# Optimization experiments

Hardware: AMD Instinct MI355X
Metric: run time of the kernel (lower is better)

## Reference

```python
import jax, jax.numpy as jnp
import numpy as np

B, T, C, H = 8, 2048, 384, 64

def setup_inputs() -> dict:
    key = jax.random.key(0)
    k1, k2, k3, k4 = jax.random.split(key, 4)
    x = jax.random.normal(k1, (B, T, C), dtype=jnp.float32)
    Wq = jax.random.normal(k2, (C, H), dtype=jnp.float32) * (C ** -0.5)
    Wk = jax.random.normal(k3, (C, H), dtype=jnp.float32) * (C ** -0.5)
    Wv = jax.random.normal(k4, (C, H), dtype=jnp.float32) * (C ** -0.5)
    return {"x": x, "Wq": Wq, "Wk": Wk, "Wv": Wv}

def reference(x, Wq, Wk, Wv):
    # x: (B, T, C); projections: (B, T, H)
    Bn, Tn, Cn = x.shape
    q = jnp.einsum('btc,ch->bth', x, Wq)
    k = jnp.einsum('btc,ch->bth', x, Wk)
    v = jnp.einsum('btc,ch->bth', x, Wv)
    # NOTE: source scales by C**-0.5 (embedding dim), not head_size**-0.5
    weights = jnp.einsum('bth,bsh->bts', q, k) * (Cn ** -0.5)  # (B, T, T)
    causal = jnp.tril(jnp.ones((Tn, Tn), dtype=bool))
    weights = jnp.where(causal, weights, -jnp.inf)
    # NOTE: source applies softmax over dim=1 (query/row axis), reproduced faithfully
    weights = jax.nn.softmax(weights, axis=1)
    # dropout omitted (eval-mode reference)
    return jnp.einsum('bts,bsh->bth', weights, v)
```

## Files before the change

### kernel.cpp

```cpp
#include <hip/hip_runtime.h>
#include <hip/hip_bf16.h>
#include <math.h>

#define Bn 8
#define Tn 2048
#define Cn 384
#define Hn 64
#define SCALE2 0.07362241f

using bf16x8 = __attribute__((ext_vector_type(8))) short;
using f32x4  = __attribute__((ext_vector_type(4))) float;
using u32x4  = __attribute__((ext_vector_type(4))) unsigned;

#define MFMA(a, b, c) __builtin_amdgcn_mfma_f32_16x16x32_bf16((a), (b), (c), 0, 0, 0)

static __device__ __forceinline__ short f2bf(float f) {
  unsigned u = __float_as_uint(f);
  u += 0x7fffu + ((u >> 16) & 1u);
  return (short)(u >> 16);
}
static __device__ __forceinline__ float bf2f(short s) {
  return __uint_as_float(((unsigned)(unsigned short)s) << 16);
}
static __device__ __forceinline__ float fexp2(float x) {
#if __has_builtin(__builtin_amdgcn_exp2f)
  return __builtin_amdgcn_exp2f(x);
#else
  return exp2f(x);
#endif
}
static __device__ __forceinline__ float frcp(float x) {
#if __has_builtin(__builtin_amdgcn_rcpf)
  return __builtin_amdgcn_rcpf(x);
#else
  return 1.0f / x;
#endif
}
static __device__ __forceinline__ unsigned pack2(float lo, float hi) {
  return (unsigned)(unsigned short)f2bf(lo) | ((unsigned)(unsigned short)f2bf(hi) << 16);
}
static __device__ __forceinline__ bf16x8 ldp(const unsigned* p) {
  u32x4 t; t[0] = p[0]; t[1] = p[1]; t[2] = p[2]; t[3] = p[3];
  return __builtin_bit_cast(bf16x8, t);
}

__global__ __launch_bounds__(256) void wconv_kernel(
    const float* __restrict__ Wq, const float* __restrict__ Wk,
    const float* __restrict__ Wv, short* __restrict__ WbT,
    float* __restrict__ Lsum) {
  int idx = blockIdx.x * 256 + threadIdx.x;
  if (idx < Bn * Tn) Lsum[idx] = 0.f;
  int n = idx / 384, k = idx - n * 384;
  const float* W = (n < 64) ? Wq : (n < 128) ? Wk : Wv;
  WbT[idx] = f2bf(W[k * 64 + (n & 63)]);
}

__global__ __launch_bounds__(256) void proj_kernel(
    const float* __restrict__ x, const short* __restrict__ WbT,
    short* __restrict__ qb, short* __restrict__ kb, short* __restrict__ vT) {
  __shared__ short xs[16][392];
  __shared__ short vtile[64][20];
  const int tid = threadIdx.x;
  const int t0 = blockIdx.x * 16;
  const float* xb = x + (size_t)t0 * Cn;
  #pragma unroll
  for (int i = 0; i < 6; ++i) {
    int j = tid + i * 256;
    int row = j / 96, colv = (j - row * 96) * 4;
    float4 v = *(const float4*)(xb + row * Cn + colv);
    short4 s4; s4.x = f2bf(v.x); s4.y = f2bf(v.y); s4.z = f2bf(v.z); s4.w = f2bf(v.w);
    *(short4*)(&xs[row][colv]) = s4;
  }
  __syncthreads();
  const int w = tid >> 6, l15 = tid & 15, quad = (tid & 63) >> 4;
  f32x4 acc[3] = {};
  for (int ks = 0; ks < 12; ++ks) {
    bf16x8 a = *(const bf16x8*)(&xs[l15][ks * 32 + quad * 8]);
    #pragma unroll
    for (int cf = 0; cf < 3; ++cf) {
      bf16x8 bfr = *(const bf16x8*)(WbT + (size_t)(48 * w + 16 * cf + l15) * Cn + ks * 32 + quad * 8);
      acc[cf] = MFMA(a, bfr, acc[cf]);
    }
  }
  #pragma unroll
  for (int cf = 0; cf < 3; ++cf) {
    int cbase = 48 * w + 16 * cf, c = cbase + l15;
    #pragma unroll
    for (int r = 0; r < 4; ++r) {
      int row = t0 + quad * 4 + r;
      short val = f2bf(acc[cf][r]);
      if (cbase < 64)       qb[(size_t)row * Hn + c] = val;
      else if (cbase < 128) kb[(size_t)row * Hn + (c - 64)] = val;
      else                  vtile[c - 128][quad * 4 + r] = val;
    }
  }
  __syncthreads();
  const int b = t0 >> 11, t0l = t0 & 2047;
  int h = tid >> 2, tseg = (tid & 3) * 4;
  *(short4*)(vT + ((size_t)(b * Hn + h)) * Tn + t0l + tseg) =
      *(const short4*)(&vtile[h][tseg]);
}

__global__ __launch_bounds__(256) void colstats_kernel(
    const short* __restrict__ qb, const short* __restrict__ kb,
    float* __restrict__ Lsum) {
  const int unit = ((blockIdx.x & 7) << 7) | (blockIdx.x >> 3);
  const int b = unit >> 7, rem = unit & 127;
  const int j = rem >> 3, u = rem & 7;
  const int lo = (u * 33) >> 3, hi = ((u + 1) * 33) >> 3;
  const int big = 32 - j;
  const int tid = threadIdx.x, w = tid >> 6, l15 = tid & 15, quad = (tid & 63) >> 4;
  __shared__ float redl[64][17];

  auto run = [&](const int i, const int k0, const int k1) {
    const int s0 = i << 6;
    float l[4] = {0.f, 0.f, 0.f, 0.f};
    const int n = k1 - k0;
    if (n > 0) {
      bf16x8 bk[8];
      #pragma unroll
      for (int nf = 0; nf < 4; ++nf) {
        const size_t krow = (size_t)(b * Tn + s0 + 16 * nf + l15) * Hn;
        bk[2 * nf]     = *(const bf16x8*)(kb + krow + quad * 8);
        bk[2 * nf + 1] = *(const bf16x8*)(kb + krow + 32 + quad * 8);
      }
      auto cload = [&](bf16x8& A0, bf16x8& A1, int k) {
        size_t ar = (size_t)(b * Tn + ((i + k) << 6) + 16 * w + l15) * Hn;
        A0 = *(const bf16x8*)(qb + ar + quad * 8);
        A1 = *(const bf16x8*)(qb + ar + 32 + quad * 8);
      };
      auto ccomp = [&](bf16x8 A0, bf16x8 A1, int k) {
        f32x4 sc[4] = {};
        #pragma unroll
        for (int nf = 0; nf < 4; ++nf) {
          sc[nf] = MFMA(A0, bk[2 * nf], sc[nf]);
          sc[nf] = MFMA(A1, bk[2 * nf + 1], sc[nf]);
        }
        const bool diag = (k == 0);
        const int tb = ((i + k) << 6) + 16 * w + quad * 4;
        #pragma unroll
        for (int nf = 0; nf < 4; ++nf) {
          int s = s0 + 16 * nf + l15;
          #pragma unroll
          for (int r = 0; r < 4; ++r) {
            float v = sc[nf][r] * SCALE2;
            if (diag && (tb + r) < s) v = -INFINITY;
            l[nf] += fexp2(v);
          }
        }
      };
      bf16x8 a0A, a1A, a0B, a1B, a0C, a1C;
      cload(a0A, a1A, k0);
      if (n > 1) cload(a0B, a1B, k0 + 1);
      if (n > 2) cload(a0C, a1C, k0 + 2);
      int k = k0;
      while (k + 3 < k1) {
        ccomp(a0A, a1A, k);     cload(a0A, a1A, k + 3);
        ccomp(a0B, a1B, k + 1); if (k + 4 < k1) cload(a0B, a1B, k + 4);
        ccomp(a0C, a1C, k + 2); if (k + 5 < k1) cload(a0C, a1C, k + 5);
        k += 3;
      }
      const int rem2 = k1 - k;
      if (rem2 > 0) ccomp(a0A, a1A, k);
      if (rem2 > 1) ccomp(a0B, a1B, k + 1);
      if (rem2 > 2) ccomp(a0C, a1C, k + 2);
    }
    __syncthreads();
    #pragma unroll
    for (int nf = 0; nf < 4; ++nf) redl[16 * nf + l15][w * 4 + quad] = l[nf];
    __syncthreads();
    if (tid < 64) {
      float ls = 0.f;
      #pragma unroll
      for (int q2 = 0; q2 < 16; ++q2) ls += redl[tid][q2];
      atomicAdd(&Lsum[b * Tn + s0 + tid], ls);
    }
  };
  run(j, lo, min(hi, big));
  run(31 - j, max(lo, big) - big, hi - big);
}

__global__ __launch_bounds__(256, 2) void outg_kernel(
    const short* __restrict__ qb, const short* __restrict__ kb,
    const short* __restrict__ vT, const float* __restrict__ Lsum,
    float* __restrict__ out) {
  const int bid = blockIdx.x;
  const int b = bid & 7;
  const int rest = bid >> 3;
  const int tile = 31 - (rest >> 1);
  const int half = rest & 1;
  const int nch = tile + 1;
  const int tid = threadIdx.x, w = tid >> 6, l15 = tid & 15, quad = (tid & 63) >> 4;
  __shared__ unsigned plds[4][512];
  __shared__ float red[4][32][64];
  __shared__ float rcpl[2048];

  const int smax = nch << 6;
  for (int s = tid; s < smax; s += 256)
    rcpl[s] = frcp(Lsum[b * Tn + s]);
  __syncthreads();

  const int swz = (l15 & 7) << 4;
  int wroff[8];
  #pragma unroll
  for (int nf = 0; nf < 4; ++nf)
    #pragma unroll
    for (int p = 0; p < 2; ++p)
      wroff[2 * nf + p] = (l15 * 128 + ((nf * 32 + quad * 8 + p * 4) ^ swz)) >> 2;
  const int rd0 = (l15 * 128 + ((quad * 16) ^ swz)) >> 2;
  const int rd1 = (l15 * 128 + ((64 + quad * 16) ^ swz)) >> 2;
  const size_t QKbase = (size_t)b * Tn * Hn;
  const size_t Vbase  = (size_t)b * Hn * Tn;
  const int tbase = (tile << 6) + (half << 5);
  const int tg0 = tbase + l15;
  const int tg1 = tbase + 16 + l15;

  const size_t qrow0 = QKbase + (size_t)(tbase + l15) * Hn;
  const size_t qrow1 = qrow0 + 16 * Hn;
  const bf16x8 qf00 = *(const bf16x8*)(qb + qrow0 + quad * 8);
  const bf16x8 qf01 = *(const bf16x8*)(qb + qrow0 + 32 + quad * 8);
  const bf16x8 qf10 = *(const bf16x8*)(qb + qrow1 + quad * 8);
  const bf16x8 qf11 = *(const bf16x8*)(qb + qrow1 + 32 + quad * 8);

  f32x4 acc0[4] = {}, acc1[4] = {};
  bf16x8 kfA[8], kfB[8], vf[8];
  auto loadK = [&](bf16x8 (&kf)[8], int ch) {
    const int s0 = ch << 6;
    #pragma unroll
    for (int nf = 0; nf < 4; ++nf) {
      const size_t kr = QKbase + (size_t)(s0 + 16 * nf + l15) * Hn;
      kf[2 * nf]     = *(const bf16x8*)(kb + kr + quad * 8);
      kf[2 * nf + 1] = *(const bf16x8*)(kb + kr + 32 + quad * 8);
    }
  };
  auto loadV = [&](int ch) {
    const int s0 = ch << 6;
    #pragma unroll
    for (int nf = 0; nf < 4; ++nf) {
      const size_t vr = Vbase + (size_t)(16 * nf + l15) * Tn + s0;
      vf[2 * nf]     = *(const bf16x8*)(vT + vr + quad * 8);
      vf[2 * nf + 1] = *(const bf16x8*)(vT + vr + 32 + quad * 8);
    }
  };
  auto strip = [&](const f32x4 (&sc)[4], const float (&rl)[16], int s0,
                   bool diag, int tg, f32x4 (&acc)[4]) {
    #pragma unroll
    for (int nf = 0; nf < 4; ++nf) {
      float ev[4];
      #pragma unroll
      for (int r = 0; r < 4; ++r) {
        float v = sc[nf][r] * SCALE2;
        const int s = s0 + 16 * nf + quad * 4 + r;
        if (diag && tg < s) v = -INFINITY;
        ev[r] = fexp2(v) * rl[nf * 4 + r];
      }
      plds[w][wroff[2 * nf]]     = pack2(ev[0], ev[1]);
      plds[w][wroff[2 * nf + 1]] = pack2(ev[2], ev[3]);
    }
    const bf16x8 a0 = ldp(&plds[w][rd0]);
    const bf16x8 a1 = ldp(&plds[w][rd1]);
    __builtin_amdgcn_s_setprio(1);
    #pragma unroll
    for (int nf = 0; nf < 4; ++nf) {
      acc[nf] = MFMA(a0, vf[2 * nf], acc[nf]);
      acc[nf] = MFMA(a1, vf[2 * nf + 1], acc[nf]);
    }
    __builtin_amdgcn_s_setprio(0);
  };
  auto body = [&](int ch, const bf16x8 (&CUR)[8], bf16x8 (&NXT)[8]) {
    const int s0 = ch << 6;
    const int nx = ch + 4;
    f32x4 sc0[4] = {}, sc1[4] = {};
    __builtin_amdgcn_s_setprio(1);
    #pragma unroll
    for (int nf = 0; nf < 4; ++nf) {
      sc0[nf] = MFMA(CUR[2 * nf], qf00, sc0[nf]);
      sc0[nf] = MFMA(CUR[2 * nf + 1], qf01, sc0[nf]);
    }
    #pragma unroll
    for (int nf = 0; nf < 4; ++nf) {
      sc1[nf] = MFMA(CUR[2 * nf], qf10, sc1[nf]);
      sc1[nf] = MFMA(CUR[2 * nf + 1], qf11, sc1[nf]);
    }
    __builtin_amdgcn_s_setprio(0);
    if (nx < nch) loadK(NXT, nx);
    float rl[16];
    #pragma unroll
    for (int nf = 0; nf < 4; ++nf)
      #pragma unroll
      for (int r = 0; r < 4; ++r)
        rl[nf * 4 + r] = rcpl[s0 + 16 * nf + quad * 4 + r];
    const bool diag = (ch == tile);
    strip(sc0, rl, s0, diag, tg0, acc0);
    strip(sc1, rl, s0, diag, tg1, acc1);
    if (nx < nch) loadV(nx);
  };

  if (w < nch) { loadK(kfA, w); loadV(w); }
  for (int ch = w; ch < nch; ch += 8) {
    body(ch, kfA, kfB);
    if (ch + 4 < nch) body(ch + 4, kfB, kfA);
  }

  #pragma unroll
  for (int nf = 0; nf < 4; ++nf)
    #pragma unroll
    for (int r = 0; r < 4; ++r) {
      red[w][quad * 4 + r][16 * nf + l15]      = acc0[nf][r];
      red[w][16 + quad * 4 + r][16 * nf + l15] = acc1[nf][r];
    }
  __syncthreads();
  {
    const int row = tid >> 3, c8 = (tid & 7) * 8;
    float4 t0 = {0.f, 0.f, 0.f, 0.f}, t1 = {0.f, 0.f, 0.f, 0.f};
    #pragma unroll
    for (int ww = 0; ww < 4; ++ww) {
      float4 s0 = *(const float4*)(&red[ww][row][c8]);
      float4 s1 = *(const float4*)(&red[ww][row][c8 + 4]);
      t0.x += s0.x; t0.y += s0.y; t0.z += s0.z; t0.w += s0.w;
      t1.x += s1.x; t1.y += s1.y; t1.z += s1.z; t1.w += s1.w;
    }
    float* o = &out[QKbase + (size_t)(tbase + row) * Hn + c8];
    *(float4*)(o) = t0;
    *(float4*)(o + 4) = t1;
  }
}

extern "C" void kernel_launch(void* const* d_in, const int* in_sizes, int n_in,
                              void* d_out, int out_size, void* d_ws, size_t ws_size,
                              hipStream_t stream) {
  const float* x  = (const float*)d_in[0];
  const float* Wq = (const float*)d_in[1];
  const float* Wk = (const float*)d_in[2];
  const float* Wv = (const float*)d_in[3];
  char* ws = (char*)d_ws;
  short* qb   = (short*)(ws);
  short* kb   = (short*)(ws + 2097152);
  short* vT   = (short*)(ws + 4194304);
  short* WbT  = (short*)(ws + 6291456);
  float* Lsum = (float*)(ws + 6438912);
  float* outp = (float*)d_out;

  hipLaunchKernelGGL(wconv_kernel, dim3(288), dim3(256), 0, stream, Wq, Wk, Wv, WbT, Lsum);
  hipLaunchKernelGGL(proj_kernel, dim3(Bn * Tn / 16), dim3(256), 0, stream, x, WbT, qb, kb, vT);
  hipLaunchKernelGGL(colstats_kernel, dim3(1024), dim3(256), 0, stream, qb, kb, Lsum);
  hipLaunchKernelGGL(outg_kernel, dim3(512), dim3(256), 0, stream, qb, kb, vT, Lsum, outp);
}
```

Measured before the change: 132.0 us.

## Fuse column-stats and output kernels via grid barrier, keeping exp scores in registers

The separate column-sum and output kernels are merged into one persistent attention kernel of 512 blocks with 512 threads. Each block computes QK^T once, keeps the bf16 exponentials in registers, reduces column sums through LDS atomics and then global atomics, waits at a software grid barrier, and does the PV pass using the stored exponentials. This avoids recomputing QK^T and exp in a second kernel and removes one launch. The softmax scale is folded into Wq during weight conversion. The cost is heavy register pressure, a grid-wide spin barrier that needs all 512 blocks resident at once (risk of deadlock or stalls), and extra bf16 rounding of unnormalized exponentials.

```diff
diff --git a/kernel.cpp b/kernel.cpp
--- a/kernel.cpp
+++ b/kernel.cpp
@@ -7,6 +7,7 @@
 #define Cn 384
 #define Hn 64
 #define SCALE2 0.07362241f
+#define NBLK 512
 
 using bf16x8 = __attribute__((ext_vector_type(8))) short;
 using f32x4  = __attribute__((ext_vector_type(4))) float;
@@ -18,9 +19,6 @@
   unsigned u = __float_as_uint(f);
   u += 0x7fffu + ((u >> 16) & 1u);
   return (short)(u >> 16);
-}
-static __device__ __forceinline__ float bf2f(short s) {
-  return __uint_as_float(((unsigned)(unsigned short)s) << 16);
 }
 static __device__ __forceinline__ float fexp2(float x) {
 #if __has_builtin(__builtin_amdgcn_exp2f)
@@ -43,16 +41,30 @@
   u32x4 t; t[0] = p[0]; t[1] = p[1]; t[2] = p[2]; t[3] = p[3];
   return __builtin_bit_cast(bf16x8, t);
 }
+static __device__ __forceinline__ void grid_barrier(unsigned* cnt) {
+  __syncthreads();
+  if (threadIdx.x == 0) {
+    __threadfence();
+    atomicAdd(cnt, 1u);
+    while (__hip_atomic_load(cnt, __ATOMIC_ACQUIRE, __HIP_MEMORY_SCOPE_AGENT)
+           < (unsigned)NBLK)
+      __builtin_amdgcn_s_sleep(8);
+  }
+  __syncthreads();
+}
 
 __global__ __launch_bounds__(256) void wconv_kernel(
     const float* __restrict__ Wq, const float* __restrict__ Wk,
     const float* __restrict__ Wv, short* __restrict__ WbT,
-    float* __restrict__ Lsum) {
+    float* __restrict__ Lsum, unsigned* __restrict__ bar) {
   int idx = blockIdx.x * 256 + threadIdx.x;
   if (idx < Bn * Tn) Lsum[idx] = 0.f;
+  if (idx == 0) *bar = 0u;
   int n = idx / 384, k = idx - n * 384;
   const float* W = (n < 64) ? Wq : (n < 128) ? Wk : Wv;
-  WbT[idx] = f2bf(W[k * 64 + (n & 63)]);
+  float wv = W[k * 64 + (n & 63)];
+  if (n < 64) wv *= SCALE2;
+  WbT[idx] = f2bf(wv);
 }
 
 __global__ __launch_bounds__(256) void proj_kernel(
@@ -101,103 +113,29 @@
       *(const short4*)(&vtile[h][tseg]);
 }
 
-__global__ __launch_bounds__(256) void colstats_kernel(
+__global__ __launch_bounds__(512, 4) void attn_kernel(
     const short* __restrict__ qb, const short* __restrict__ kb,
-    float* __restrict__ Lsum) {
-  const int unit = ((blockIdx.x & 7) << 7) | (blockIdx.x >> 3);
-  const int b = unit >> 7, rem = unit & 127;
-  const int j = rem >> 3, u = rem & 7;
-  const int lo = (u * 33) >> 3, hi = ((u + 1) * 33) >> 3;
-  const int big = 32 - j;
-  const int tid = threadIdx.x, w = tid >> 6, l15 = tid & 15, quad = (tid & 63) >> 4;
-  __shared__ float redl[64][17];
-
-  auto run = [&](const int i, const int k0, const int k1) {
-    const int s0 = i << 6;
-    float l[4] = {0.f, 0.f, 0.f, 0.f};
-    const int n = k1 - k0;
-    if (n > 0) {
-      bf16x8 bk[8];
-      #pragma unroll
-      for (int nf = 0; nf < 4; ++nf) {
-        const size_t krow = (size_t)(b * Tn + s0 + 16 * nf + l15) * Hn;
-        bk[2 * nf]     = *(const bf16x8*)(kb + krow + quad * 8);
-        bk[2 * nf + 1] = *(const bf16x8*)(kb + krow + 32 + quad * 8);
-      }
-      auto cload = [&](bf16x8& A0, bf16x8& A1, int k) {
-        size_t ar = (size_t)(b * Tn + ((i + k) << 6) + 16 * w + l15) * Hn;
-        A0 = *(const bf16x8*)(qb + ar + quad * 8);
-        A1 = *(const bf16x8*)(qb + ar + 32 + quad * 8);
-      };
-      auto ccomp = [&](bf16x8 A0, bf16x8 A1, int k) {
-        f32x4 sc[4] = {};
-        #pragma unroll
-        for (int nf = 0; nf < 4; ++nf) {
-          sc[nf] = MFMA(A0, bk[2 * nf], sc[nf]);
-          sc[nf] = MFMA(A1, bk[2 * nf + 1], sc[nf]);
-        }
-        const bool diag = (k == 0);
-        const int tb = ((i + k) << 6) + 16 * w + quad * 4;
-        #pragma unroll
-        for (int nf = 0; nf < 4; ++nf) {
-          int s = s0 + 16 * nf + l15;
-          #pragma unroll
-          for (int r = 0; r < 4; ++r) {
-            float v = sc[nf][r] * SCALE2;
-            if (diag && (tb + r) < s) v = -INFINITY;
-            l[nf] += fexp2(v);
-          }
-        }
-      };
-      bf16x8 a0A, a1A, a0B, a1B, a0C, a1C;
-      cload(a0A, a1A, k0);
-      if (n > 1) cload(a0B, a1B, k0 + 1);
-      if (n > 2) cload(a0C, a1C, k0 + 2);
-      int k = k0;
-      while (k + 3 < k1) {
-        ccomp(a0A, a1A, k);     cload(a0A, a1A, k + 3);
-        ccomp(a0B, a1B, k + 1); if (k + 4 < k1) cload(a0B, a1B, k + 4);
-        ccomp(a0C, a1C, k + 2); if (k + 5 < k1) cload(a0C, a1C, k + 5);
-        k += 3;
-      }
-      const int rem2 = k1 - k;
-      if (rem2 > 0) ccomp(a0A, a1A, k);
-      if (rem2 > 1) ccomp(a0B, a1B, k + 1);
-      if (rem2 > 2) ccomp(a0C, a1C, k + 2);
-    }
-    __syncthreads();
-    #pragma unroll
-    for (int nf = 0; nf < 4; ++nf) redl[16 * nf + l15][w * 4 + quad] = l[nf];
-    __syncthreads();
-    if (tid < 64) {
-      float ls = 0.f;
-      #pragma unroll
-      for (int q2 = 0; q2 < 16; ++q2) ls += redl[tid][q2];
-      atomicAdd(&Lsum[b * Tn + s0 + tid], ls);
-    }
-  };
-  run(j, lo, min(hi, big));
-  run(31 - j, max(lo, big) - big, hi - big);
-}
-
-__global__ __launch_bounds__(256, 2) void outg_kernel(
-    const short* __restrict__ qb, const short* __restrict__ kb,
-    const short* __restrict__ vT, const float* __restrict__ Lsum,
-    float* __restrict__ out) {
+    const short* __restrict__ vT, float* __restrict__ Lsum,
+    unsigned* __restrict__ bar, float* __restrict__ out) {
+  __shared__ alignas(16) float lsum_lds[2048];
+  __shared__ alignas(16) unsigned plds[8][512];
+  __shared__ alignas(16) float red[4][32][64];
+
   const int bid = blockIdx.x;
   const int b = bid & 7;
-  const int rest = bid >> 3;
-  const int tile = 31 - (rest >> 1);
-  const int half = rest & 1;
-  const int nch = tile + 1;
-  const int tid = threadIdx.x, w = tid >> 6, l15 = tid & 15, quad = (tid & 63) >> 4;
-  __shared__ unsigned plds[4][512];
-  __shared__ float red[4][32][64];
-  __shared__ float rcpl[2048];
-
-  const int smax = nch << 6;
-  for (int s = tid; s < smax; s += 256)
-    rcpl[s] = frcp(Lsum[b * Tn + s]);
+  const int r_ = bid >> 3;
+  const int j = r_ >> 2;
+  const int quarter = r_ & 3;
+  const int tA = j, tB = 31 - j;
+  const int tid = threadIdx.x;
+  const int w = tid >> 6, l15 = tid & 15, quad = (tid & 63) >> 4;
+  const int lo = (w * 33) >> 3, hi = ((w + 1) * 33) >> 3;
+  const int tb0 = (tA << 6) + (quarter << 4);
+  const int tb1 = (tB << 6) + (quarter << 4);
+  const size_t QKbase = (size_t)b * Tn * Hn;
+  const size_t Vbase  = (size_t)b * Hn * Tn;
+
+  for (int s = tid; s < 2048; s += 512) lsum_lds[s] = 0.f;
   __syncthreads();
 
   const int swz = (l15 & 7) << 4;
@@ -209,22 +147,11 @@
       wroff[2 * nf + p] = (l15 * 128 + ((nf * 32 + quad * 8 + p * 4) ^ swz)) >> 2;
   const int rd0 = (l15 * 128 + ((quad * 16) ^ swz)) >> 2;
   const int rd1 = (l15 * 128 + ((64 + quad * 16) ^ swz)) >> 2;
-  const size_t QKbase = (size_t)b * Tn * Hn;
-  const size_t Vbase  = (size_t)b * Hn * Tn;
-  const int tbase = (tile << 6) + (half << 5);
-  const int tg0 = tbase + l15;
-  const int tg1 = tbase + 16 + l15;
-
-  const size_t qrow0 = QKbase + (size_t)(tbase + l15) * Hn;
-  const size_t qrow1 = qrow0 + 16 * Hn;
-  const bf16x8 qf00 = *(const bf16x8*)(qb + qrow0 + quad * 8);
-  const bf16x8 qf01 = *(const bf16x8*)(qb + qrow0 + 32 + quad * 8);
-  const bf16x8 qf10 = *(const bf16x8*)(qb + qrow1 + quad * 8);
-  const bf16x8 qf11 = *(const bf16x8*)(qb + qrow1 + 32 + quad * 8);
-
-  f32x4 acc0[4] = {}, acc1[4] = {};
-  bf16x8 kfA[8], kfB[8], vf[8];
-  auto loadK = [&](bf16x8 (&kf)[8], int ch) {
+
+  auto chOf = [&](int g) { return (g > tA) ? (g - tA - 1) : g; };
+
+  bf16x8 kf[8], vf[8];
+  auto loadK = [&](int ch) {
     const int s0 = ch << 6;
     #pragma unroll
     for (int nf = 0; nf < 4; ++nf) {
@@ -242,87 +169,136 @@
       vf[2 * nf + 1] = *(const bf16x8*)(vT + vr + 32 + quad * 8);
     }
   };
-  auto strip = [&](const f32x4 (&sc)[4], const float (&rl)[16], int s0,
-                   bool diag, int tg, f32x4 (&acc)[4]) {
-    #pragma unroll
-    for (int nf = 0; nf < 4; ++nf) {
-      float ev[4];
+
+  unsigned Ereg[5][8];
+  loadK(chOf(lo));
+  #pragma unroll
+  for (int i = 0; i < 5; ++i) {
+    const int g = lo + i;
+    if (g < hi) {
+      const int ch = chOf(g);
+      const int tbase = (g > tA) ? tb1 : tb0;
+      const bool diag = (ch == ((g > tA) ? tB : tA));
+      const size_t qrow = QKbase + (size_t)(tbase + l15) * Hn;
+      const bf16x8 qf0 = *(const bf16x8*)(qb + qrow + quad * 8);
+      const bf16x8 qf1 = *(const bf16x8*)(qb + qrow + 32 + quad * 8);
+      f32x4 sc[4] = {};
+      __builtin_amdgcn_s_setprio(1);
       #pragma unroll
-      for (int r = 0; r < 4; ++r) {
-        float v = sc[nf][r] * SCALE2;
-        const int s = s0 + 16 * nf + quad * 4 + r;
-        if (diag && tg < s) v = -INFINITY;
-        ev[r] = fexp2(v) * rl[nf * 4 + r];
+      for (int nf = 0; nf < 4; ++nf) {
+        sc[nf] = MFMA(kf[2 * nf], qf0, sc[nf]);
+        sc[nf] = MFMA(kf[2 * nf + 1], qf1, sc[nf]);
       }
-      plds[w][wroff[2 * nf]]     = pack2(ev[0], ev[1]);
-      plds[w][wroff[2 * nf + 1]] = pack2(ev[2], ev[3]);
-    }
-    const bf16x8 a0 = ldp(&plds[w][rd0]);
-    const bf16x8 a1 = ldp(&plds[w][rd1]);
-    __builtin_amdgcn_s_setprio(1);
-    #pragma unroll
-    for (int nf = 0; nf < 4; ++nf) {
-      acc[nf] = MFMA(a0, vf[2 * nf], acc[nf]);
-      acc[nf] = MFMA(a1, vf[2 * nf + 1], acc[nf]);
-    }
-    __builtin_amdgcn_s_setprio(0);
+      __builtin_amdgcn_s_setprio(0);
+      if (g + 1 < hi) loadK(chOf(g + 1));
+      const int tg = tbase + l15;
+      #pragma unroll
+      for (int nf = 0; nf < 4; ++nf) {
+        f32x4 ev;
+        if (diag) {
+          #pragma unroll
+          for (int r = 0; r < 4; ++r) {
+            const int s = (ch << 6) + 16 * nf + 4 * quad + r;
+            ev[r] = fexp2((tg < s) ? -INFINITY : sc[nf][r]);
+          }
+        } else {
+          #pragma unroll
+          for (int r = 0; r < 4; ++r) ev[r] = fexp2(sc[nf][r]);
+        }
+        Ereg[i][2 * nf]     = pack2(ev[0], ev[1]);
+        Ereg[i][2 * nf + 1] = pack2(ev[2], ev[3]);
+        #pragma unroll
+        for (int m = 1; m < 16; m <<= 1)
+          #pragma unroll
+          for (int r = 0; r < 4; ++r)
+            ev[r] += __shfl_xor(ev[r], m, 16);
+        if (l15 == 0) {
+          #pragma unroll
+          for (int r = 0; r < 4; ++r)
+            atomicAdd(&lsum_lds[(ch << 6) + 16 * nf + 4 * quad + r], ev[r]);
+        }
+      }
+    }
+  }
+  __syncthreads();
+  for (int s = tid; s < 2048; s += 512)
+    atomicAdd(&Lsum[b * Tn + s], lsum_lds[s]);
+  grid_barrier(bar);
+  for (int s = tid; s < 2048; s += 512)
+    lsum_lds[s] = frcp(__hip_atomic_load(&Lsum[b * Tn + s],
+                                         __ATOMIC_RELAXED,
+                                         __HIP_MEMORY_SCOPE_AGENT));
+  __syncthreads();
+
+  f32x4 acc[4];
+  auto pvpass = [&](bool stripB) {
+    #pragma unroll
+    for (int nf = 0; nf < 4; ++nf) acc[nf] = f32x4{0.f, 0.f, 0.f, 0.f};
+    const int g0 = stripB ? ((lo > tA + 1) ? lo : tA + 1) : lo;
+    const int g1 = stripB ? hi : ((hi < tA + 1) ? hi : tA + 1);
+    if (g0 < g1) loadV(chOf(g0));
+    #pragma unroll
+    for (int i = 0; i < 5; ++i) {
+      const int g = lo + i;
+      if (g >= g0 && g < g1) {
+        const int ch = chOf(g);
+        #pragma unroll
+        for (int nf = 0; nf < 4; ++nf) {
+          float4 rl4 = *(const float4*)&lsum_lds[(ch << 6) + 16 * nf + 4 * quad];
+          unsigned e01 = Ereg[i][2 * nf], e23 = Ereg[i][2 * nf + 1];
+          float p0 = __uint_as_float(e01 << 16) * rl4.x;
+          float p1 = __uint_as_float(e01 & 0xffff0000u) * rl4.y;
+          float p2 = __uint_as_float(e23 << 16) * rl4.z;
+          float p3 = __uint_as_float(e23 & 0xffff0000u) * rl4.w;
+          plds[w][wroff[2 * nf]]     = pack2(p0, p1);
+          plds[w][wroff[2 * nf + 1]] = pack2(p2, p3);
+        }
+        const bf16x8 a0 = ldp(&plds[w][rd0]);
+        const bf16x8 a1 = ldp(&plds[w][rd1]);
+        __builtin_amdgcn_s_setprio(1);
+        #pragma unroll
+        for (int nf = 0; nf < 4; ++nf) {
+          acc[nf] = MFMA(a0, vf[2 * nf], acc[nf]);
+          acc[nf] = MFMA(a1, vf[2 * nf + 1], acc[nf]);
+        }
+        __builtin_amdgcn_s_setprio(0);
+        if (g + 1 < g1) loadV(chOf(g + 1));
+      }
+    }
+    const int rb = stripB ? 16 : 0;
+    if (w < 4) {
+      #pragma unroll
+      for (int nf = 0; nf < 4; ++nf)
+        #pragma unroll
+        for (int r = 0; r < 4; ++r)
+          red[w][rb + quad * 4 + r][16 * nf + l15] = acc[nf][r];
+    }
+    __syncthreads();
+    if (w >= 4) {
+      #pragma unroll
+      for (int nf = 0; nf < 4; ++nf)
+        #pragma unroll
+        for (int r = 0; r < 4; ++r)
+          red[w - 4][rb + quad * 4 + r][16 * nf + l15] += acc[nf][r];
+    }
+    __syncthreads();
   };
-  auto body = [&](int ch, const bf16x8 (&CUR)[8], bf16x8 (&NXT)[8]) {
-    const int s0 = ch << 6;
-    const int nx = ch + 4;
-    f32x4 sc0[4] = {}, sc1[4] = {};
-    __builtin_amdgcn_s_setprio(1);
-    #pragma unroll
-    for (int nf = 0; nf < 4; ++nf) {
-      sc0[nf] = MFMA(CUR[2 * nf], qf00, sc0[nf]);
-      sc0[nf] = MFMA(CUR[2 * nf + 1], qf01, sc0[nf]);
-    }
-    #pragma unroll
-    for (int nf = 0; nf < 4; ++nf) {
-      sc1[nf] = MFMA(CUR[2 * nf], qf10, sc1[nf]);
-      sc1[nf] = MFMA(CUR[2 * nf + 1], qf11, sc1[nf]);
-    }
-    __builtin_amdgcn_s_setprio(0);
-    if (nx < nch) loadK(NXT, nx);
-    float rl[16];
-    #pragma unroll
-    for (int nf = 0; nf < 4; ++nf)
-      #pragma unroll
-      for (int r = 0; r < 4; ++r)
-        rl[nf * 4 + r] = rcpl[s0 + 16 * nf + quad * 4 + r];
-    const bool diag = (ch == tile);
-    strip(sc0, rl, s0, diag, tg0, acc0);
-    strip(sc1, rl, s0, diag, tg1, acc1);
-    if (nx < nch) loadV(nx);
-  };
-
-  if (w < nch) { loadK(kfA, w); loadV(w); }
-  for (int ch = w; ch < nch; ch += 8) {
-    body(ch, kfA, kfB);
-    if (ch + 4 < nch) body(ch + 4, kfB, kfA);
-  }
-
-  #pragma unroll
-  for (int nf = 0; nf < 4; ++nf)
-    #pragma unroll
-    for (int r = 0; r < 4; ++r) {
-      red[w][quad * 4 + r][16 * nf + l15]      = acc0[nf][r];
-      red[w][16 + quad * 4 + r][16 * nf + l15] = acc1[nf][r];
-    }
-  __syncthreads();
+  pvpass(false);
+  pvpass(true);
+
   {
-    const int row = tid >> 3, c8 = (tid & 7) * 8;
-    float4 t0 = {0.f, 0.f, 0.f, 0.f}, t1 = {0.f, 0.f, 0.f, 0.f};
-    #pragma unroll
-    for (int ww = 0; ww < 4; ++ww) {
-      float4 s0 = *(const float4*)(&red[ww][row][c8]);
-      float4 s1 = *(const float4*)(&red[ww][row][c8 + 4]);
-      t0.x += s0.x; t0.y += s0.y; t0.z += s0.z; t0.w += s0.w;
-      t1.x += s1.x; t1.y += s1.y; t1.z += s1.z; t1.w += s1.w;
-    }
-    float* o = &out[QKbase + (size_t)(tbase + row) * Hn + c8];
-    *(float4*)(o) = t0;
-    *(float4*)(o + 4) = t1;
+    const int row = tid >> 4, c4 = (tid & 15) * 4;
+    float4 s0 = *(const float4*)(&red[0][row][c4]);
+    float4 s1 = *(const float4*)(&red[1][row][c4]);
+    float4 s2 = *(const float4*)(&red[2][row][c4]);
+    float4 s3 = *(const float4*)(&red[3][row][c4]);
+    float4 t;
+    t.x = (s0.x + s1.x) + (s2.x + s3.x);
+    t.y = (s0.y + s1.y) + (s2.y + s3.y);
+    t.z = (s0.z + s1.z) + (s2.z + s3.z);
+    t.w = (s0.w + s1.w) + (s2.w + s3.w);
+    const int trow = (row < 16) ? (tb0 + row) : (tb1 + row - 16);
+    *(float4*)(&out[QKbase + (size_t)trow * Hn + c4]) = t;
   }
 }
 
@@ -339,10 +315,10 @@
   short* vT   = (short*)(ws + 4194304);
   short* WbT  = (short*)(ws + 6291456);
   float* Lsum = (float*)(ws + 6438912);
+  unsigned* bar = (unsigned*)(ws + 6504448);
   float* outp = (float*)d_out;
 
-  hipLaunchKernelGGL(wconv_kernel, dim3(288), dim3(256), 0, stream, Wq, Wk, Wv, WbT, Lsum);
+  hipLaunchKernelGGL(wconv_kernel, dim3(288), dim3(256), 0, stream, Wq, Wk, Wv, WbT, Lsum, bar);
   hipLaunchKernelGGL(proj_kernel, dim3(Bn * Tn / 16), dim3(256), 0, stream, x, WbT, qb, kb, vT);
-  hipLaunchKernelGGL(colstats_kernel, dim3(1024), dim3(256), 0, stream, qb, kb, Lsum);
-  hipLaunchKernelGGL(outg_kernel, dim3(512), dim3(256), 0, stream, qb, kb, vT, Lsum, outp);
-}
+  hipLaunchKernelGGL(attn_kernel, dim3(NBLK), dim3(512), 0, stream, qb, kb, vT, Lsum, bar, outp);
+}
```

Measured after the change: 187.5 us. +42.1%, slower.
